# Optimization experiments

Measured on AMD Instinct MI355X. Metric: run time of the kernel, lower is better.

The kernel has to match this reference:

```python
import jax, jax.numpy as jnp
import numpy as np

PS = 7          # window_size
HEADS = 8
DIM = 64
EPS = 1e-12     # F.normalize default eps


def resize_bilinear(x, oh, ow, align_corners):
    """PyTorch-style bilinear resize for NCHW tensors (antialias=False)."""
    b, c, h, w = x.shape
    if align_corners:
        ys = jnp.linspace(0.0, h - 1.0, oh, dtype=x.dtype)
        xs = jnp.linspace(0.0, w - 1.0, ow, dtype=x.dtype)
    else:
        ys = jnp.maximum((jnp.arange(oh, dtype=x.dtype) + 0.5) * (h / oh) - 0.5, 0.0)
        xs = jnp.maximum((jnp.arange(ow, dtype=x.dtype) + 0.5) * (w / ow) - 0.5, 0.0)
    y0 = jnp.floor(ys).astype(jnp.int32)
    x0 = jnp.floor(xs).astype(jnp.int32)
    y1 = jnp.minimum(y0 + 1, h - 1)
    x1 = jnp.minimum(x0 + 1, w - 1)
    ly = (ys - y0.astype(x.dtype))[None, None, :, None]   # (1,1,oh,1)
    lx = (xs - x0.astype(x.dtype))[None, None, None, :]   # (1,1,1,ow)
    rows = x[:, :, y0, :] * (1.0 - ly) + x[:, :, y1, :] * ly       # (b,c,oh,w)
    out = rows[:, :, :, x0] * (1.0 - lx) + rows[:, :, :, x1] * lx  # (b,c,oh,ow)
    return out


def _to_windows(t, b, heads, d, ps, xb, yb):
    # 'b (head d) (x h ph) (y w pw) -> (b x y) head d (w ph) (pw h)'
    t = t.reshape(b, heads, d, xb, ps, ps, yb, ps, ps)  # b,head,d,x,h,ph,y,w,pw
    t = t.transpose(0, 3, 6, 1, 2, 7, 5, 8, 4)          # b,x,y,head,d,w,ph,pw,h
    return t.reshape(b * xb * yb, heads, d, ps * ps, ps * ps)


def _from_windows(t, b, heads, d, ps, xb, yb):
    # inverse rearrange back to (b, head*d, x*ps*ps, y*ps*ps)
    t = t.reshape(b, xb, yb, heads, d, ps, ps, ps, ps)  # b,x,y,head,d,w,ph,pw,h
    t = t.transpose(0, 3, 4, 1, 8, 6, 2, 5, 7)          # b,head,d,x,h,ph,y,w,pw
    return t.reshape(b, heads * d, xb * ps * ps, yb * ps * ps)


def setup_inputs() -> dict:
    key = jax.random.key(0)
    k1, k2, k3, k4 = jax.random.split(key, 4)
    x = jax.random.normal(k1, (4, DIM, 256, 256), jnp.float32)
    qkv_w = jax.random.normal(k2, (3 * DIM, DIM), jnp.float32) * 0.05
    dw_w = jax.random.normal(k3, (3 * DIM, 1, 3, 3), jnp.float32) * 0.05
    proj_w = jax.random.normal(k4, (DIM, DIM), jnp.float32) * 0.05
    return {"x": x, "qkv_w": qkv_w, "dw_w": dw_w, "proj_w": proj_w}


def reference(x, qkv_w, dw_w, proj_w):
    b, c, h, w = x.shape
    heads, ps = HEADS, PS
    ps2 = ps * ps
    temph = -(-h // ps2) * ps2   # next multiple of ps^2 (matches while loop)
    tempw = -(-w // ps2) * ps2
    d = c // heads

    # conv1x1 (qkv) then depthwise 3x3 conv
    qkv = jnp.einsum('bchw,oc->bohw', x, qkv_w)
    qkv = jax.lax.conv_general_dilated(
        qkv, dw_w, window_strides=(1, 1), padding=((1, 1), (1, 1)),
        feature_group_count=3 * c,
        dimension_numbers=('NCHW', 'OIHW', 'NCHW'))

    # pad by bilinear interpolation, align_corners=True
    qkv = resize_bilinear(qkv, temph, tempw, align_corners=True)
    q, k, v = jnp.split(qkv, 3, axis=1)

    xb, yb = temph // ps2, tempw // ps2
    q = _to_windows(q, b, heads, d, ps, xb, yb)  # (b*xb*yb, heads, d, 49, 49)
    k = _to_windows(k, b, heads, d, ps, xb, yb)
    v = _to_windows(v, b, heads, d, ps, xb, yb)

    # L2-normalized (cosine) attention along the last axis, no temperature
    qn = q / jnp.maximum(jnp.linalg.norm(q, axis=-1, keepdims=True), EPS)
    kn = k / jnp.maximum(jnp.linalg.norm(k, axis=-1, keepdims=True), EPS)
    attn = jax.nn.softmax(qn @ jnp.swapaxes(kn, -1, -2), axis=-1)
    out = attn @ v

    out = _from_windows(out, b, heads, d, ps, xb, yb)
    out = resize_bilinear(out, h, w, align_corners=False)
    return jnp.einsum('bchw,oc->bohw', out, proj_w)
```

## Files before the change

kernel.cpp:

```cpp
#include <hip/hip_runtime.h>
#include <math.h>

#define BATCH 4
#define CIN 64
#define HW 256
#define NPIX 65536
#define OC 192
#define TH 294
#define NPIX_R 86436
#define PS2 49
#define C2N 2401
#define NWIN 36
#define WCPB 2304
#define KSTR 52
#define TABN (NWIN * C2N)

__device__ __forceinline__ float rl_f32(float v, int lane) {
    return __uint_as_float(__builtin_amdgcn_readlane(__float_as_uint(v), lane));
}

__global__ __launch_bounds__(256)
void k_qkv1x1(const float* __restrict__ x, const float* __restrict__ w,
              float* __restrict__ A) {
    __shared__ float wT[64][64];
    __shared__ float xs[64][256];
    x += (size_t)blockIdx.z * CIN * NPIX;
    A += (size_t)blockIdx.z * OC * NPIX;
    const int tid = threadIdx.x;
    const int pxbase = blockIdx.x * 256;
    const int ocbase = blockIdx.y * 64;

    for (int idx = tid; idx < 1024; idx += 256) {
        int o = idx >> 4, c4 = idx & 15;
        float4 v = *reinterpret_cast<const float4*>(w + (size_t)(ocbase + o) * CIN + c4 * 4);
        wT[c4 * 4 + 0][o] = v.x; wT[c4 * 4 + 1][o] = v.y;
        wT[c4 * 4 + 2][o] = v.z; wT[c4 * 4 + 3][o] = v.w;
    }
    for (int idx = tid; idx < 4096; idx += 256) {
        int c = idx >> 6, p4 = idx & 63;
        float4 v = *reinterpret_cast<const float4*>(x + (size_t)c * NPIX + pxbase + p4 * 4);
        *reinterpret_cast<float4*>(&xs[c][p4 * 4]) = v;
    }
    __syncthreads();

    const int tx = tid & 15, ty = tid >> 4;
    float acc[4][16];
    #pragma unroll
    for (int a = 0; a < 4; ++a)
        #pragma unroll
        for (int b = 0; b < 16; ++b) acc[a][b] = 0.f;

    #pragma unroll 4
    for (int k = 0; k < 64; ++k) {
        float4 wv = *reinterpret_cast<const float4*>(&wT[k][ty * 4]);
        float wr[4] = {wv.x, wv.y, wv.z, wv.w};
        float xv[16];
        #pragma unroll
        for (int i = 0; i < 4; ++i) {
            float4 v = *reinterpret_cast<const float4*>(&xs[k][tx * 4 + i * 64]);
            xv[i * 4 + 0] = v.x; xv[i * 4 + 1] = v.y;
            xv[i * 4 + 2] = v.z; xv[i * 4 + 3] = v.w;
        }
        #pragma unroll
        for (int a = 0; a < 4; ++a)
            #pragma unroll
            for (int b = 0; b < 16; ++b)
                acc[a][b] = fmaf(wr[a], xv[b], acc[a][b]);
    }

    #pragma unroll
    for (int a = 0; a < 4; ++a) {
        float* Ap = A + (size_t)(ocbase + ty * 4 + a) * NPIX + pxbase;
        #pragma unroll
        for (int i = 0; i < 4; ++i)
            *reinterpret_cast<float4*>(Ap + tx * 4 + i * 64) =
                make_float4(acc[a][i * 4 + 0], acc[a][i * 4 + 1],
                            acc[a][i * 4 + 2], acc[a][i * 4 + 3]);
    }
}

__global__ __launch_bounds__(256)
void k_dw3x3(const float* __restrict__ A, const float* __restrict__ dwv,
             float* __restrict__ Bf) {
    A  += (size_t)blockIdx.z * OC * NPIX;
    Bf += (size_t)blockIdx.z * OC * NPIX;
    int gid = blockIdx.x * 256 + threadIdx.x;
    int ch = gid >> 13;
    int q  = gid & 8191;
    int y  = q >> 5;
    int x8 = (q & 31) << 3;
    const float* Ap = A + (size_t)ch * NPIX;
    float wv[9];
    #pragma unroll
    for (int i = 0; i < 9; ++i) wv[i] = dwv[ch * 9 + i];
    float a[8];
    #pragma unroll
    for (int t = 0; t < 8; ++t) a[t] = 0.f;
    #pragma unroll
    for (int ky = 0; ky < 3; ++ky) {
        int yy = y + ky - 1;
        if (yy < 0 || yy >= HW) continue;
        const float* row = Ap + yy * HW;
        float4 m0 = *reinterpret_cast<const float4*>(row + x8);
        float4 m1 = *reinterpret_cast<const float4*>(row + x8 + 4);
        float lm = (x8 > 0)       ? row[x8 - 1] : 0.f;
        float rp = (x8 < HW - 8)  ? row[x8 + 8] : 0.f;
        float cv[10] = {lm, m0.x, m0.y, m0.z, m0.w, m1.x, m1.y, m1.z, m1.w, rp};
        #pragma unroll
        for (int kx = 0; kx < 3; ++kx) {
            float wk = wv[ky * 3 + kx];
            #pragma unroll
            for (int t = 0; t < 8; ++t)
                a[t] = fmaf(cv[t + kx], wk, a[t]);
        }
    }
    float* op = Bf + (size_t)ch * NPIX + y * HW + x8;
    *reinterpret_cast<float4*>(op)     = make_float4(a[0], a[1], a[2], a[3]);
    *reinterpret_cast<float4*>(op + 4) = make_float4(a[4], a[5], a[6], a[7]);
}

__global__ __launch_bounds__(256)
void k_prep(int4* __restrict__ itab, float4* __restrict__ wtab,
            int* __restrict__ dtab, int* __restrict__ otab) {
    const int w = blockIdx.x;
    const int xw = w / 6, yw = w - xw * 6;
    const float scale = 255.0f / 293.0f;
    for (int e = threadIdx.x; e < C2N; e += 256) {
        int rl = e / PS2, cl = e - rl * PS2;
        float sy = (float)(xw * PS2 + rl) * scale;
        float sx = (float)(yw * PS2 + cl) * scale;
        int y0 = (int)sy, x0 = (int)sx;
        float ly = sy - y0, lx = sx - x0;
        int y1 = min(y0 + 1, HW - 1), x1 = min(x0 + 1, HW - 1);
        itab[w * C2N + e] = make_int4(y0 * HW + x0, y0 * HW + x1,
                                      y1 * HW + x0, y1 * HW + x1);
        wtab[w * C2N + e] = make_float4((1.f - ly) * (1.f - lx), (1.f - ly) * lx,
                                        ly * (1.f - lx),         ly * lx);
        if (w == 0) {
            int i = (cl / 7) * 7 + rl % 7;
            int j = (cl % 7) * 7 + rl / 7;
            dtab[e] = i * KSTR + j;
            otab[e] = rl * TH + cl;
        }
    }
}

#define PIN4(v) asm volatile("" : "+v"(v.x), "+v"(v.y), "+v"(v.z), "+v"(v.w))
#define SQ4(v) fmaf(v.x, v.x, fmaf(v.y, v.y, fmaf(v.z, v.z, v.w * v.w)))
#define DOT4(KV, OFS) { float4 q_ = *reinterpret_cast<const float4*>(qr + (OFS)); \
    dd0 = fmaf(q_.x, KV.x, dd0); dd1 = fmaf(q_.y, KV.y, dd1); \
    dd2 = fmaf(q_.z, KV.z, dd2); dd3 = fmaf(q_.w, KV.w, dd3); }
#define PV4(VV, J) { \
    o0 = fmaf(rl_f32(p, (J)+0), VV.x, o0); o1 = fmaf(rl_f32(p, (J)+1), VV.y, o1); \
    o2 = fmaf(rl_f32(p, (J)+2), VV.z, o2); o3 = fmaf(rl_f32(p, (J)+3), VV.w, o3); }
#define VC(jj) (act ? Vs[(jj) * KSTR + l] : 1.0f)

__global__ __launch_bounds__(256, 2)
void k_attn(const float* __restrict__ Bf,
            const int4* __restrict__ itab, const float4* __restrict__ wtab,
            const int* __restrict__ dtab, const int* __restrict__ otab,
            float* __restrict__ Cf) {
    __shared__ float Qs[PS2 * KSTR];
    __shared__ float Ks[PS2 * KSTR];
    __shared__ float Vs[PS2 * KSTR];
    Bf += (size_t)blockIdx.z * OC * NPIX;
    Cf += (size_t)blockIdx.z * (size_t)CIN * NPIX_R;
    const int tid = threadIdx.x;
    const int wv = tid >> 6, lane = tid & 63;
    const int wc  = blockIdx.x;
    const int ch  = wc & 63;
    const int win = wc >> 6;
    const int xw  = win / 6, yw = win - xw * 6;
    const float* qb = Bf + (size_t)ch * NPIX;
    const float* kb = qb + (size_t)64  * NPIX;
    const float* vb = qb + (size_t)128 * NPIX;
    const int wbase = win * C2N;

    for (int e = tid; e < C2N; e += 256) {
        int4   o  = itab[wbase + e];
        float4 wt = wtab[wbase + e];
        int    d  = dtab[e];
        Qs[d] = qb[o.x] * wt.x + qb[o.y] * wt.y + qb[o.z] * wt.z + qb[o.w] * wt.w;
        Ks[d] = kb[o.x] * wt.x + kb[o.y] * wt.y + kb[o.z] * wt.z + kb[o.w] * wt.w;
        Vs[d] = vb[o.x] * wt.x + vb[o.y] * wt.y + vb[o.z] * wt.z + vb[o.w] * wt.w;
    }
    __syncthreads();

    const int l = min(lane, PS2 - 1);
    const bool act = (lane < PS2);

    const float* kr0 = &Ks[l * KSTR];
    float4 k0  = *reinterpret_cast<const float4*>(kr0 + 0);
    float4 k1  = *reinterpret_cast<const float4*>(kr0 + 4);
    float4 k2  = *reinterpret_cast<const float4*>(kr0 + 8);
    float4 k3  = *reinterpret_cast<const float4*>(kr0 + 12);
    float4 k4  = *reinterpret_cast<const float4*>(kr0 + 16);
    float4 k5  = *reinterpret_cast<const float4*>(kr0 + 20);
    float4 k6  = *reinterpret_cast<const float4*>(kr0 + 24);
    float4 k7  = *reinterpret_cast<const float4*>(kr0 + 28);
    float4 k8  = *reinterpret_cast<const float4*>(kr0 + 32);
    float4 k9  = *reinterpret_cast<const float4*>(kr0 + 36);
    float4 k10 = *reinterpret_cast<const float4*>(kr0 + 40);
    float4 k11 = *reinterpret_cast<const float4*>(kr0 + 44);
    float  k48 = kr0[48];
    PIN4(k0); PIN4(k1); PIN4(k2); PIN4(k3); PIN4(k4); PIN4(k5);
    PIN4(k6); PIN4(k7); PIN4(k8); PIN4(k9); PIN4(k10); PIN4(k11);

    float kss = SQ4(k0) + SQ4(k1) + SQ4(k2) + SQ4(k3) + SQ4(k4) + SQ4(k5)
              + SQ4(k6) + SQ4(k7) + SQ4(k8) + SQ4(k9) + SQ4(k10) + SQ4(k11)
              + k48 * k48;
    const float inkl = 1.f / fmaxf(sqrtf(kss), 1e-12f);

    float4 v0  = make_float4(VC(0),  VC(1),  VC(2),  VC(3));
    float4 v1  = make_float4(VC(4),  VC(5),  VC(6),  VC(7));
    float4 v2  = make_float4(VC(8),  VC(9),  VC(10), VC(11));
    float4 v3  = make_float4(VC(12), VC(13), VC(14), VC(15));
    float4 v4  = make_float4(VC(16), VC(17), VC(18), VC(19));
    float4 v5  = make_float4(VC(20), VC(21), VC(22), VC(23));
    float4 v6  = make_float4(VC(24), VC(25), VC(26), VC(27));
    float4 v7  = make_float4(VC(28), VC(29), VC(30), VC(31));
    float4 v8  = make_float4(VC(32), VC(33), VC(34), VC(35));
    float4 v9  = make_float4(VC(36), VC(37), VC(38), VC(39));
    float4 v10 = make_float4(VC(40), VC(41), VC(42), VC(43));
    float4 v11 = make_float4(VC(44), VC(45), VC(46), VC(47));
    float  v48 = VC(48);
    PIN4(v0); PIN4(v1); PIN4(v2); PIN4(v3); PIN4(v4); PIN4(v5);
    PIN4(v6); PIN4(v7); PIN4(v8); PIN4(v9); PIN4(v10); PIN4(v11);
    asm volatile("" : "+v"(k48), "+v"(v48));

    float inql;
    {
        const float* qrl = &Qs[l * KSTR];
        float qss = 0.f;
        #pragma unroll
        for (int u = 0; u < 12; ++u) {
            float4 t = *reinterpret_cast<const float4*>(qrl + u * 4);
            qss += SQ4(t);
        }
        float q48 = qrl[48];
        qss = fmaf(q48, q48, qss);
        inql = 1.f / fmaxf(sqrtf(qss), 1e-12f);
    }
    __syncthreads();

    for (int i = wv; i < PS2; i += 4) {
        const float inq_i = rl_f32(inql, i);
        const float* qr = &Qs[i * KSTR];
        float dd0 = 0.f, dd1 = 0.f, dd2 = 0.f, dd3 = 0.f;
        DOT4(k0, 0)   DOT4(k1, 4)   DOT4(k2, 8)   DOT4(k3, 12)
        DOT4(k4, 16)  DOT4(k5, 20)  DOT4(k6, 24)  DOT4(k7, 28)
        DOT4(k8, 32)  DOT4(k9, 36)  DOT4(k10, 40) DOT4(k11, 44)
        float dsum = (dd0 + dd1) + (dd2 + dd3);
        dsum = fmaf(qr[48], k48, dsum);
        float p = __expf(dsum * inkl * inq_i);

        float o0 = 0.f, o1 = 0.f, o2 = 0.f, o3 = 0.f;
        PV4(v0, 0)   PV4(v1, 4)   PV4(v2, 8)   PV4(v3, 12)
        PV4(v4, 16)  PV4(v5, 20)  PV4(v6, 24)  PV4(v7, 28)
        PV4(v8, 32)  PV4(v9, 36)  PV4(v10, 40) PV4(v11, 44)
        float ot = (o0 + o1) + (o2 + o3);
        ot = fmaf(rl_f32(p, 48), v48, ot);
        float ssum = rl_f32(ot, 49);
        float res = ot * __builtin_amdgcn_rcpf(ssum);
        if (act) Qs[i * KSTR + lane] = res;
    }
    __syncthreads();

    float* cb = Cf + (size_t)ch * NPIX_R + (xw * PS2) * TH + yw * PS2;
    for (int e = tid; e < C2N; e += 256)
        cb[otab[e]] = Qs[dtab[e]];
}

__global__ __launch_bounds__(256)
void k_down(const float* __restrict__ Cf, float* __restrict__ D) {
    Cf += (size_t)blockIdx.z * (size_t)CIN * NPIX_R;
    D  += (size_t)blockIdx.z * (size_t)CIN * NPIX;
    int gid = blockIdx.x * 256 + threadIdx.x;
    int ch = gid >> 14;
    int q  = gid & 16383;
    int y  = q >> 6;
    int x4 = (q & 63) << 2;
    const float sc = 294.0f / 256.0f;
    float sy = fmaxf((y + 0.5f) * sc - 0.5f, 0.f);
    int y0 = (int)sy;
    float ly = sy - y0;
    int y1 = min(y0 + 1, TH - 1);
    const float* r0 = Cf + (size_t)ch * NPIX_R + y0 * TH;
    const float* r1 = Cf + (size_t)ch * NPIX_R + y1 * TH;
    float res[4];
    #pragma unroll
    for (int t = 0; t < 4; ++t) {
        float sx = fmaxf((x4 + t + 0.5f) * sc - 0.5f, 0.f);
        int x0 = (int)sx;
        float lx = sx - x0;
        int x1 = min(x0 + 1, TH - 1);
        res[t] = (r0[x0] * (1.f - lx) + r0[x1] * lx) * (1.f - ly)
               + (r1[x0] * (1.f - lx) + r1[x1] * lx) * ly;
    }
    *reinterpret_cast<float4*>(D + (size_t)ch * NPIX + y * HW + x4) =
        make_float4(res[0], res[1], res[2], res[3]);
}

__global__ __launch_bounds__(256)
void k_pmm(const float* __restrict__ D, const float* __restrict__ w,
           float* __restrict__ out) {
    __shared__ float wT[64][64];
    __shared__ float xs[64][256];
    D   += (size_t)blockIdx.z * CIN * NPIX;
    out += (size_t)blockIdx.z * CIN * NPIX;
    const int tid = threadIdx.x;
    const int pxbase = blockIdx.x * 256;

    for (int idx = tid; idx < 1024; idx += 256) {
        int o = idx >> 4, c4 = idx & 15;
        float4 v = *reinterpret_cast<const float4*>(w + (size_t)o * CIN + c4 * 4);
        wT[c4 * 4 + 0][o] = v.x; wT[c4 * 4 + 1][o] = v.y;
        wT[c4 * 4 + 2][o] = v.z; wT[c4 * 4 + 3][o] = v.w;
    }
    for (int idx = tid; idx < 4096; idx += 256) {
        int c = idx >> 6, p4 = idx & 63;
        float4 v = *reinterpret_cast<const float4*>(D + (size_t)c * NPIX + pxbase + p4 * 4);
        *reinterpret_cast<float4*>(&xs[c][p4 * 4]) = v;
    }
    __syncthreads();

    const int tx = tid & 15, ty = tid >> 4;
    float acc[4][16];
    #pragma unroll
    for (int a = 0; a < 4; ++a)
        #pragma unroll
        for (int b = 0; b < 16; ++b) acc[a][b] = 0.f;

    #pragma unroll 4
    for (int k = 0; k < 64; ++k) {
        float4 wv = *reinterpret_cast<const float4*>(&wT[k][ty * 4]);
        float wr[4] = {wv.x, wv.y, wv.z, wv.w};
        float xv[16];
        #pragma unroll
        for (int i = 0; i < 4; ++i) {
            float4 v = *reinterpret_cast<const float4*>(&xs[k][tx * 4 + i * 64]);
            xv[i * 4 + 0] = v.x; xv[i * 4 + 1] = v.y;
            xv[i * 4 + 2] = v.z; xv[i * 4 + 3] = v.w;
        }
        #pragma unroll
        for (int a = 0; a < 4; ++a)
            #pragma unroll
            for (int b = 0; b < 16; ++b)
                acc[a][b] = fmaf(wr[a], xv[b], acc[a][b]);
    }

    #pragma unroll
    for (int a = 0; a < 4; ++a) {
        float* op = out + (size_t)(ty * 4 + a) * NPIX + pxbase;
        #pragma unroll
        for (int i = 0; i < 4; ++i)
            *reinterpret_cast<float4*>(op + tx * 4 + i * 64) =
                make_float4(acc[a][i * 4 + 0], acc[a][i * 4 + 1],
                            acc[a][i * 4 + 2], acc[a][i * 4 + 3]);
    }
}

extern "C" void kernel_launch(void* const* d_in, const int* in_sizes, int n_in,
                              void* d_out, int out_size, void* d_ws, size_t ws_size,
                              hipStream_t stream) {
    const float* x   = (const float*)d_in[0];
    const float* qw  = (const float*)d_in[1];
    const float* dwv = (const float*)d_in[2];
    const float* pw  = (const float*)d_in[3];
    float* out = (float*)d_out;

    const size_t perAB = (size_t)OC * NPIX;
    const size_t needBig = (size_t)2 * BATCH * perAB * sizeof(float);
    const size_t needMid = (size_t)2 * 2 * perAB * sizeof(float);

    int NB;
    if (ws_size >= needBig)      NB = BATCH;
    else if (ws_size >= needMid) NB = 2;
    else                         NB = 1;

    float* A = (float*)d_ws;
    float* B = A + (size_t)NB * perAB;
    float* C = A;
    float* D = A + (size_t)NB * CIN * NPIX_R;
    float* T = A + (size_t)NB * (CIN * NPIX_R + CIN * NPIX);
    int4*   itab = (int4*)T;
    float4* wtab = (float4*)(T + (size_t)TABN * 4);
    int*    dtab = (int*)(T + (size_t)TABN * 8);
    int*    otab = dtab + C2N;

    for (int b = 0; b < BATCH; b += NB) {
        const float* xb = x + (size_t)b * CIN * NPIX;
        float* ob = out + (size_t)b * CIN * NPIX;
        hipLaunchKernelGGL(k_qkv1x1, dim3(256, 3, NB),  dim3(256), 0, stream, xb, qw, A);
        hipLaunchKernelGGL(k_dw3x3,  dim3(6144, 1, NB), dim3(256), 0, stream, A, dwv, B);
        hipLaunchKernelGGL(k_prep,   dim3(NWIN, 1, 1),  dim3(256), 0, stream,
                           itab, wtab, dtab, otab);
        hipLaunchKernelGGL(k_attn,   dim3(WCPB, 1, NB), dim3(256), 0, stream,
                           B, itab, wtab, dtab, otab, C);
        hipLaunchKernelGGL(k_down,   dim3(4096, 1, NB), dim3(256), 0, stream, C, D);
        hipLaunchKernelGGL(k_pmm,    dim3(256, 1, NB),  dim3(256), 0, stream, D, pw, ob);
    }
}
```

Before: 558.3 us.

## Fuse bilinear downsample into projection matmul and unroll attention gather loop

Result: faster. 511.5 us (-8.4%).

```diff
diff --git a/kernel.cpp b/kernel.cpp
--- a/kernel.cpp
+++ b/kernel.cpp
@@ -154,6 +154,13 @@
     o0 = fmaf(rl_f32(p, (J)+0), VV.x, o0); o1 = fmaf(rl_f32(p, (J)+1), VV.y, o1); \
     o2 = fmaf(rl_f32(p, (J)+2), VV.z, o2); o3 = fmaf(rl_f32(p, (J)+3), VV.w, o3); }
 #define VC(jj) (act ? Vs[(jj) * KSTR + l] : 1.0f)
+#define GBODY(E) { \
+    int4   o_  = itab[wbase + (E)]; \
+    float4 wt_ = wtab[wbase + (E)]; \
+    int    d_  = dtab[(E)]; \
+    Qs[d_] = qb[o_.x] * wt_.x + qb[o_.y] * wt_.y + qb[o_.z] * wt_.z + qb[o_.w] * wt_.w; \
+    Ks[d_] = kb[o_.x] * wt_.x + kb[o_.y] * wt_.y + kb[o_.z] * wt_.z + kb[o_.w] * wt_.w; \
+    Vs[d_] = vb[o_.x] * wt_.x + vb[o_.y] * wt_.y + vb[o_.z] * wt_.z + vb[o_.w] * wt_.w; }
 
 __global__ __launch_bounds__(256, 2)
 void k_attn(const float* __restrict__ Bf,
@@ -176,13 +183,13 @@
     const float* vb = qb + (size_t)128 * NPIX;
     const int wbase = win * C2N;
 
-    for (int e = tid; e < C2N; e += 256) {
-        int4   o  = itab[wbase + e];
-        float4 wt = wtab[wbase + e];
-        int    d  = dtab[e];
-        Qs[d] = qb[o.x] * wt.x + qb[o.y] * wt.y + qb[o.z] * wt.z + qb[o.w] * wt.w;
-        Ks[d] = kb[o.x] * wt.x + kb[o.y] * wt.y + kb[o.z] * wt.z + kb[o.w] * wt.w;
-        Vs[d] = vb[o.x] * wt.x + vb[o.y] * wt.y + vb[o.z] * wt.z + vb[o.w] * wt.w;
+    #pragma unroll 3
+    for (int it = 0; it < 9; ++it) {
+        int e = tid + it * 256;
+        GBODY(e)
+    }
+    if (tid < C2N - 2304) {
+        GBODY(2304 + tid)
     }
     __syncthreads();
 
@@ -272,44 +279,25 @@
 }
 
 __global__ __launch_bounds__(256)
-void k_down(const float* __restrict__ Cf, float* __restrict__ D) {
-    Cf += (size_t)blockIdx.z * (size_t)CIN * NPIX_R;
-    D  += (size_t)blockIdx.z * (size_t)CIN * NPIX;
-    int gid = blockIdx.x * 256 + threadIdx.x;
-    int ch = gid >> 14;
-    int q  = gid & 16383;
-    int y  = q >> 6;
-    int x4 = (q & 63) << 2;
+void k_downpmm(const float* __restrict__ Cf, const float* __restrict__ w,
+               float* __restrict__ out) {
+    __shared__ float wT[64][64];
+    __shared__ float xs[64][256];
+    Cf  += (size_t)blockIdx.z * (size_t)CIN * NPIX_R;
+    out += (size_t)blockIdx.z * CIN * NPIX;
+    const int tid = threadIdx.x;
+    const int y = blockIdx.x;
     const float sc = 294.0f / 256.0f;
     float sy = fmaxf((y + 0.5f) * sc - 0.5f, 0.f);
     int y0 = (int)sy;
     float ly = sy - y0;
     int y1 = min(y0 + 1, TH - 1);
-    const float* r0 = Cf + (size_t)ch * NPIX_R + y0 * TH;
-    const float* r1 = Cf + (size_t)ch * NPIX_R + y1 * TH;
-    float res[4];
-    #pragma unroll
-    for (int t = 0; t < 4; ++t) {
-        float sx = fmaxf((x4 + t + 0.5f) * sc - 0.5f, 0.f);
-        int x0 = (int)sx;
-        float lx = sx - x0;
-        int x1 = min(x0 + 1, TH - 1);
-        res[t] = (r0[x0] * (1.f - lx) + r0[x1] * lx) * (1.f - ly)
-               + (r1[x0] * (1.f - lx) + r1[x1] * lx) * ly;
-    }
-    *reinterpret_cast<float4*>(D + (size_t)ch * NPIX + y * HW + x4) =
-        make_float4(res[0], res[1], res[2], res[3]);
-}
-
-__global__ __launch_bounds__(256)
-void k_pmm(const float* __restrict__ D, const float* __restrict__ w,
-           float* __restrict__ out) {
-    __shared__ float wT[64][64];
-    __shared__ float xs[64][256];
-    D   += (size_t)blockIdx.z * CIN * NPIX;
-    out += (size_t)blockIdx.z * CIN * NPIX;
-    const int tid = threadIdx.x;
-    const int pxbase = blockIdx.x * 256;
+    float sx = fmaxf((tid + 0.5f) * sc - 0.5f, 0.f);
+    int x0 = (int)sx;
+    float lx = sx - x0;
+    int x1 = min(x0 + 1, TH - 1);
+    const float w00 = (1.f - ly) * (1.f - lx), w01 = (1.f - ly) * lx;
+    const float w10 = ly * (1.f - lx),         w11 = ly * lx;
 
     for (int idx = tid; idx < 1024; idx += 256) {
         int o = idx >> 4, c4 = idx & 15;
@@ -317,10 +305,11 @@
         wT[c4 * 4 + 0][o] = v.x; wT[c4 * 4 + 1][o] = v.y;
         wT[c4 * 4 + 2][o] = v.z; wT[c4 * 4 + 3][o] = v.w;
     }
-    for (int idx = tid; idx < 4096; idx += 256) {
-        int c = idx >> 6, p4 = idx & 63;
-        float4 v = *reinterpret_cast<const float4*>(D + (size_t)c * NPIX + pxbase + p4 * 4);
-        *reinterpret_cast<float4*>(&xs[c][p4 * 4]) = v;
+    #pragma unroll 4
+    for (int ch = 0; ch < 64; ++ch) {
+        const float* r0 = Cf + (size_t)ch * NPIX_R + y0 * TH;
+        const float* r1 = Cf + (size_t)ch * NPIX_R + y1 * TH;
+        xs[ch][tid] = r0[x0] * w00 + r0[x1] * w01 + r1[x0] * w10 + r1[x1] * w11;
     }
     __syncthreads();
 
@@ -351,7 +340,7 @@
 
     #pragma unroll
     for (int a = 0; a < 4; ++a) {
-        float* op = out + (size_t)(ty * 4 + a) * NPIX + pxbase;
+        float* op = out + (size_t)(ty * 4 + a) * NPIX + y * HW;
         #pragma unroll
         for (int i = 0; i < 4; ++i)
             *reinterpret_cast<float4*>(op + tx * 4 + i * 64) =
@@ -381,8 +370,7 @@
     float* A = (float*)d_ws;
     float* B = A + (size_t)NB * perAB;
     float* C = A;
-    float* D = A + (size_t)NB * CIN * NPIX_R;
-    float* T = A + (size_t)NB * (CIN * NPIX_R + CIN * NPIX);
+    float* T = A + (size_t)NB * CIN * NPIX_R;
     int4*   itab = (int4*)T;
     float4* wtab = (float4*)(T + (size_t)TABN * 4);
     int*    dtab = (int*)(T + (size_t)TABN * 8);
@@ -391,13 +379,12 @@
     for (int b = 0; b < BATCH; b += NB) {
         const float* xb = x + (size_t)b * CIN * NPIX;
         float* ob = out + (size_t)b * CIN * NPIX;
-        hipLaunchKernelGGL(k_qkv1x1, dim3(256, 3, NB),  dim3(256), 0, stream, xb, qw, A);
-        hipLaunchKernelGGL(k_dw3x3,  dim3(6144, 1, NB), dim3(256), 0, stream, A, dwv, B);
-        hipLaunchKernelGGL(k_prep,   dim3(NWIN, 1, 1),  dim3(256), 0, stream,
+        hipLaunchKernelGGL(k_qkv1x1,  dim3(256, 3, NB),  dim3(256), 0, stream, xb, qw, A);
+        hipLaunchKernelGGL(k_dw3x3,   dim3(6144, 1, NB), dim3(256), 0, stream, A, dwv, B);
+        hipLaunchKernelGGL(k_prep,    dim3(NWIN, 1, 1),  dim3(256), 0, stream,
                            itab, wtab, dtab, otab);
-        hipLaunchKernelGGL(k_attn,   dim3(WCPB, 1, NB), dim3(256), 0, stream,
+        hipLaunchKernelGGL(k_attn,    dim3(WCPB, 1, NB), dim3(256), 0, stream,
                            B, itab, wtab, dtab, otab, C);
-        hipLaunchKernelGGL(k_down,   dim3(4096, 1, NB), dim3(256), 0, stream, C, D);
-        hipLaunchKernelGGL(k_pmm,    dim3(256, 1, NB),  dim3(256), 0, stream, D, pw, ob);
-    }
-}
+        hipLaunchKernelGGL(k_downpmm, dim3(256, 1, NB),  dim3(256), 0, stream, C, pw, ob);
+    }
+}
```
